# Performance work log

Hardware: AMD Instinct MI355X
Metric: run time of the kernel (lower is better)

## Reference

```python
import jax, jax.numpy as jnp
import numpy as np

B, NV, NC, D, E = 16, 8192, 4096, 128, 49152


def _gru_cell(x, h, w_ih, w_hh, b_ih, b_hh):
    """torch.nn.GRUCell math; gate order r, z, n; weights are (3D, D)."""
    gi = x @ w_ih.T + b_ih
    gh = h @ w_hh.T + b_hh
    ir, iz, inn = jnp.split(gi, 3, axis=-1)
    hr, hz, hn = jnp.split(gh, 3, axis=-1)
    r = jax.nn.sigmoid(ir + hr)
    z = jax.nn.sigmoid(iz + hz)
    n = jnp.tanh(inn + r * hn)
    return (1.0 - z) * n + z * h


def _msg_net(x, w1, b1, w2, b2):
    # Linear -> exact GELU -> Linear (torch nn.GELU default is erf-based)
    return jax.nn.gelu(x @ w1.T + b1, approximate=False) @ w2.T + b2


def _spmm(feats, src_idx, dst_idx, n_out):
    """Binary sparse-matrix @ dense: gather rows at src_idx, segment-sum to dst_idx.
    feats: (B, N_src, D) -> (B, n_out, D). Equivalent to torch.sparse.mm(H, feats[i])."""
    gathered = feats[:, src_idx, :]  # (B, E, D)
    return jax.vmap(lambda g: jax.ops.segment_sum(g, dst_idx, num_segments=n_out))(gathered)


def setup_inputs() -> dict:
    key = jax.random.key(0)
    ks = jax.random.split(key, 20)
    s = 0.05
    inp = {
        "v_feats": jax.random.normal(ks[0], (B, NV, D), jnp.float32),
        "c_feats": jax.random.normal(ks[1], (B, NC, D), jnp.float32),
        "edge_chk": jax.random.randint(ks[2], (E,), 0, NC, jnp.int32),
        "edge_var": jax.random.randint(ks[3], (E,), 0, NV, jnp.int32),
        # msg_net: Linear(D,D) -> GELU -> Linear(D,D)
        "msg_w1": jax.random.normal(ks[4], (D, D), jnp.float32) * s,
        "msg_b1": jnp.zeros((D,), jnp.float32),
        "msg_w2": jax.random.normal(ks[5], (D, D), jnp.float32) * s,
        "msg_b2": jnp.zeros((D,), jnp.float32),
        # var_update GRUCell(D, D)
        "var_w_ih": jax.random.normal(ks[6], (3 * D, D), jnp.float32) * s,
        "var_w_hh": jax.random.normal(ks[7], (3 * D, D), jnp.float32) * s,
        "var_b_ih": jnp.zeros((3 * D,), jnp.float32),
        "var_b_hh": jnp.zeros((3 * D,), jnp.float32),
        # chk_update GRUCell(D, D)
        "chk_w_ih": jax.random.normal(ks[8], (3 * D, D), jnp.float32) * s,
        "chk_w_hh": jax.random.normal(ks[9], (3 * D, D), jnp.float32) * s,
        "chk_b_ih": jnp.zeros((3 * D,), jnp.float32),
        "chk_b_hh": jnp.zeros((3 * D,), jnp.float32),
    }
    return inp


def reference(v_feats, c_feats, edge_chk, edge_var,
              msg_w1, msg_b1, msg_w2, msg_b2,
              var_w_ih, var_w_hh, var_b_ih, var_b_hh,
              chk_w_ih, chk_w_hh, chk_b_ih, chk_b_hh):
    b, nv, d = v_feats.shape
    nc = c_feats.shape[1]
    # variable -> check: H @ v_feats (H is binary, rows=checks, cols=vars)
    v_to_c = _spmm(v_feats, edge_var, edge_chk, nc)        # (B, NC, D)
    v_to_c = _msg_net(v_to_c, msg_w1, msg_b1, msg_w2, msg_b2)
    c_new = _gru_cell(v_to_c.reshape(-1, d), c_feats.reshape(-1, d),
                      chk_w_ih, chk_w_hh, chk_b_ih, chk_b_hh).reshape(b, nc, d)
    # check -> variable: H^T @ c_new
    c_to_v = _spmm(c_new, edge_chk, edge_var, nv)          # (B, NV, D)
    c_to_v = _msg_net(c_to_v, msg_w1, msg_b1, msg_w2, msg_b2)
    v_new = _gru_cell(c_to_v.reshape(-1, d), v_feats.reshape(-1, d),
                      var_w_ih, var_w_hh, var_b_ih, var_b_hh).reshape(b, nv, d)
    return (v_new, c_new)
```

## Files before the change

kernel.cpp:

```cpp
#include <hip/hip_runtime.h>

using u16 = unsigned short;
using u32 = unsigned int;
using u64 = unsigned long long;
typedef short short8 __attribute__((ext_vector_type(8)));
typedef unsigned short ushort8 __attribute__((ext_vector_type(8)));
typedef float f32x4 __attribute__((ext_vector_type(4)));

#define GB  16
#define GNV 8192
#define GNC 4096
#define GD  128
#define GE  49152

#define MFMA __builtin_amdgcn_mfma_f32_16x16x32_bf16


__device__ __forceinline__ u16 f2bf(float f){
    u32 u = __builtin_bit_cast(u32, f);
    u32 r = (u >> 16) & 1u;
    u += 0x7fffu + r;
    return (u16)(u >> 16);
}

__device__ __forceinline__ float bf2f(u16 x){
    return __builtin_bit_cast(float, (u32)x << 16);
}

__device__ __forceinline__ u64 pack4(float a, float b, float c, float d){
    return (u64)f2bf(a) | ((u64)f2bf(b) << 16) | ((u64)f2bf(c) << 32) | ((u64)f2bf(d) << 48);
}

__device__ __forceinline__ float sigmoidf_(float x){
    return __fdividef(1.f, 1.f + __expf(-x));
}

__device__ __forceinline__ float tanhf_fast(float x){
    float xc = fminf(15.f, fmaxf(-15.f, x));
    float t  = __expf(2.f * xc);
    return __fdividef(t - 1.f, t + 1.f);
}

__device__ __forceinline__ char* swzp(const void* base, int row, int bc){
    return (char*)base + row * 256 + (bc ^ ((row & 7) << 4));
}

__device__ __forceinline__ short8 ldfrag(const u16* tile, int row, int lane, int ks){
    int bc = ks * 64 + ((lane >> 4) << 4);
    return *(const short8*)swzp(tile, row, bc);
}


__global__ void k_hist(const int* __restrict__ ec, const int* __restrict__ ev,
                       int* cc, int* cv){
    int e = blockIdx.x * 256 + threadIdx.x;
    if (e < GE){ atomicAdd(&cc[ec[e]], 1); atomicAdd(&cv[ev[e]], 1); }
}

__global__ __launch_bounds__(1024) void k_scan(const int* __restrict__ cnt, int* off, int n){
    __shared__ int part[1024];
    int tid = threadIdx.x;
    int chunk = n >> 10;
    int base = tid * chunk;
    int s = 0;
    for (int i = 0; i < chunk; ++i) s += cnt[base + i];
    part[tid] = s;
    __syncthreads();
    #pragma unroll
    for (int ofs = 1; ofs < 1024; ofs <<= 1){
        int v = (tid >= ofs) ? part[tid - ofs] : 0;
        __syncthreads();
        part[tid] += v;
        __syncthreads();
    }
    if (tid == 1023) off[n] = part[1023];
    int run = part[tid] - s;
    for (int i = 0; i < chunk; ++i){ off[base + i] = run; run += cnt[base + i]; }
}

__global__ void k_fill(const int* __restrict__ ec, const int* __restrict__ ev,
                       int* cur_c, int* lst_c, int* cur_v, int* lst_v){
    int e = blockIdx.x * 256 + threadIdx.x;
    if (e < GE){
        int c = ec[e], v = ev[e];
        lst_c[atomicAdd(&cur_c[c], 1)] = v;
        lst_v[atomicAdd(&cur_v[v], 1)] = c;
    }
}

__global__ void k_sort(const int* __restrict__ off, int* lst, int n){
    int i = blockIdx.x * 256 + threadIdx.x;
    if (i >= n) return;
    int s = off[i], e = off[i + 1];
    for (int a = s + 1; a < e; ++a){
        int v = lst[a]; int b = a - 1;
        while (b >= s && lst[b] > v){ lst[b + 1] = lst[b]; --b; }
        lst[b + 1] = v;
    }
}

__global__ void k_cvt(const float* __restrict__ s, u16* d, int n){
    int i = blockIdx.x * 256 + threadIdx.x;
    if (i < n) d[i] = f2bf(s[i]);
}


__global__ __launch_bounds__(256) void k_tr(const float* __restrict__ src,
                                            u16* __restrict__ dstT, int n){
    const int node = blockIdx.x, t = threadIdx.x;
    const int b = t >> 4, d0 = (t & 15) * 8;
    const float4* s = (const float4*)(src + ((size_t)b * n + node) * GD + d0);
    float4 v0 = s[0], v1 = s[1];
    u64* p = (u64*)(dstT + (size_t)node * 2048 + t * 8);
    p[0] = pack4(v0.x, v0.y, v0.z, v0.w);
    p[1] = pack4(v1.x, v1.y, v1.z, v1.w);
}


__global__ __launch_bounds__(256) void k_spmm(const u16* __restrict__ srcT,
                                              const int* __restrict__ off,
                                              const int* __restrict__ lst,
                                              u16* __restrict__ dst, int ndst){
    const int node = blockIdx.x, t = threadIdx.x;
    const int b = t >> 4, d0 = (t & 15) * 8;
    float acc[8];
    #pragma unroll
    for (int i = 0; i < 8; ++i) acc[i] = 0.f;
    const int s = off[node], e = off[node + 1];
    const u16* base = srcT + t * 8;
    for (int a = s; a < e; ++a){
        ushort8 v = *(const ushort8*)(base + (size_t)lst[a] * 2048);
        #pragma unroll
        for (int i = 0; i < 8; ++i) acc[i] += bf2f(v[i]);
    }
    u64* p = (u64*)(dst + ((size_t)b * ndst + node) * GD + d0);
    p[0] = pack4(acc[0], acc[1], acc[2], acc[3]);
    p[1] = pack4(acc[4], acc[5], acc[6], acc[7]);
}


__global__ __launch_bounds__(512, 2) void k_msg(u16* __restrict__ X,
                                                const u16* __restrict__ W1, const float* __restrict__ b1,
                                                const u16* __restrict__ W2, const float* __restrict__ b2,
                                                int ntiles){
    __shared__ __align__(16) u16 Xs[2][64 * 128];
    __shared__ __align__(16) u16 Gs[64 * 128];
    const int tid = threadIdx.x, lane = tid & 63, w = tid >> 6;
    const int l15 = lane & 15, rg = lane >> 4;
    const int j = w * 16 + l15;

    short8 w1f[4], w2f[4];
    #pragma unroll
    for (int ks = 0; ks < 4; ++ks){
        w1f[ks] = *(const short8*)(W1 + (size_t)j * 128 + ks * 32 + rg * 8);
        w2f[ks] = *(const short8*)(W2 + (size_t)j * 128 + ks * 32 + rg * 8);
    }
    const float bb1 = b1[j], bb2 = b2[j];

    const int nk = ntiles / gridDim.x;
    u64 xr[4];
    auto issue = [&](int tt){
        const u64* xs = (const u64*)(X + (size_t)tt * 64 * 128);
        #pragma unroll
        for (int i = 0; i < 4; ++i) xr[i] = xs[tid + i * 512];
    };

    issue(blockIdx.x);
    for (int k = 0; k < nk; ++k){
        const int buf = k & 1;
        #pragma unroll
        for (int i = 0; i < 4; ++i){
            int idx = tid + i * 512;
            *(u64*)swzp(Xs[buf], idx >> 5, (idx & 31) << 3) = xr[i];
        }
        __syncthreads();
        if (k + 1 < nk) issue(blockIdx.x + (k + 1) * gridDim.x);

        #pragma unroll
        for (int sub = 0; sub < 4; ++sub){
            const u16* xt = Xs[buf] + sub * 16 * 128;
            f32x4 acc = {0, 0, 0, 0};
            #pragma unroll
            for (int ks = 0; ks < 4; ++ks)
                acc = MFMA(ldfrag(xt, l15, lane, ks), w1f[ks], acc, 0, 0, 0);
            #pragma unroll
            for (int i = 0; i < 4; ++i){
                float v = acc[i] + bb1;
                float g = 0.5f * v * (1.f + erff(v * 0.70710678f));
                *(u16*)swzp(Gs, sub * 16 + rg * 4 + i, j * 2) = f2bf(g);
            }
        }
        __syncthreads();

        const size_t row0 = (size_t)(blockIdx.x + (size_t)k * gridDim.x) * 64;
        #pragma unroll
        for (int sub = 0; sub < 4; ++sub){
            const u16* gt = Gs + sub * 16 * 128;
            f32x4 acc = {0, 0, 0, 0};
            #pragma unroll
            for (int ks = 0; ks < 4; ++ks)
                acc = MFMA(ldfrag(gt, l15, lane, ks), w2f[ks], acc, 0, 0, 0);
            #pragma unroll
            for (int i = 0; i < 4; ++i)
                X[(row0 + sub * 16 + rg * 4 + i) * GD + j] = f2bf(acc[i] + bb2);
        }
    }
}


__global__ __launch_bounds__(512, 2) void k_gru(const u16* __restrict__ Xb, const float* __restrict__ Hf,
                                                const u16* __restrict__ Wih, const float* __restrict__ bih,
                                                const u16* __restrict__ Whh, const float* __restrict__ bhh,
                                                float* __restrict__ Out, u16* __restrict__ OutT,
                                                int logN, int ntiles){
    __shared__ __align__(16) u16  Xs[2][64 * 128];
    __shared__ __align__(16) u16  Hs[2][64 * 128];
    __shared__ __align__(16) float Hraw[2][64 * 128];
    const int tid = threadIdx.x, lane = tid & 63, w = tid >> 6;
    const int l15 = lane & 15, rg = lane >> 4;
    const int j = w * 16 + l15;
    const int nmask = (1 << logN) - 1;

    short8 wf[6][4];
    #pragma unroll
    for (int g = 0; g < 3; ++g){
        #pragma unroll
        for (int ks = 0; ks < 4; ++ks){
            wf[g][ks]     = *(const short8*)(Wih + (size_t)(g * 128 + j) * 128 + ks * 32 + rg * 8);
            wf[g + 3][ks] = *(const short8*)(Whh + (size_t)(g * 128 + j) * 128 + ks * 32 + rg * 8);
        }
    }
    const float bir = bih[j]       + bhh[j];
    const float biz = bih[128 + j] + bhh[128 + j];
    const float bin = bih[256 + j];
    const float bhn = bhh[256 + j];

    const int nk = ntiles / gridDim.x;
    u64 xr[4]; float4 hr[4];

    auto issue = [&](int t){
        const u64*    xs = (const u64*)   (Xb + (size_t)t * 64 * 128);
        const float4* hs = (const float4*)(Hf + (size_t)t * 64 * 128);
        #pragma unroll
        for (int i = 0; i < 4; ++i){ xr[i] = xs[tid + i * 512]; hr[i] = hs[tid + i * 512]; }
    };

    issue(blockIdx.x);
    for (int k = 0; k < nk; ++k){
        const int buf = k & 1;
        #pragma unroll
        for (int i = 0; i < 4; ++i){
            int idx = tid + i * 512;
            int row = idx >> 5, c8 = idx & 31;
            *(u64*)swzp(Xs[buf], row, c8 << 3) = xr[i];
            float4 v = hr[i];
            *(float4*)&Hraw[buf][row * 128 + c8 * 4] = v;
            *(u64*)swzp(Hs[buf], row, c8 << 3) = pack4(v.x, v.y, v.z, v.w);
        }
        __syncthreads();
        if (k + 1 < nk) issue(blockIdx.x + (k + 1) * gridDim.x);

        const int row0 = (blockIdx.x + k * gridDim.x) * 64;
        #pragma unroll
        for (int sub = 0; sub < 4; ++sub){
            const u16* xt = Xs[buf] + sub * 16 * 128;
            const u16* ht = Hs[buf] + sub * 16 * 128;
            f32x4 ar = {0,0,0,0}, az = {0,0,0,0}, an = {0,0,0,0}, hn = {0,0,0,0};
            #pragma unroll
            for (int ks = 0; ks < 4; ++ks){
                short8 a = ldfrag(xt, l15, lane, ks);
                short8 h = ldfrag(ht, l15, lane, ks);
                ar = MFMA(a, wf[0][ks], ar, 0, 0, 0);
                az = MFMA(a, wf[1][ks], az, 0, 0, 0);
                an = MFMA(a, wf[2][ks], an, 0, 0, 0);
                ar = MFMA(h, wf[3][ks], ar, 0, 0, 0);
                az = MFMA(h, wf[4][ks], az, 0, 0, 0);
                hn = MFMA(h, wf[5][ks], hn, 0, 0, 0);
            }
            #pragma unroll
            for (int i = 0; i < 4; ++i){
                int r = sub * 16 + rg * 4 + i;
                float h0 = Hraw[buf][r * 128 + j];
                float rr = sigmoidf_(ar[i] + bir);
                float zz = sigmoidf_(az[i] + biz);
                float nn = tanhf_fast(an[i] + bin + rr * (hn[i] + bhn));
                float val = (1.f - zz) * nn + zz * h0;
                int rg_ = row0 + r;
                Out[(size_t)rg_ * GD + j] = val;
                if (OutT){
                    int bidx = rg_ >> logN, node = rg_ & nmask;
                    OutT[(((size_t)node << 4) + bidx) * GD + j] = f2bf(val);
                }
            }
        }
        __syncthreads();
    }
}


extern "C" void kernel_launch(void* const* d_in, const int* in_sizes, int n_in,
                              void* d_out, int out_size, void* d_ws, size_t ws_size,
                              hipStream_t stream){
    const float* v_feats  = (const float*)d_in[0];
    const float* c_feats  = (const float*)d_in[1];
    const int*   edge_chk = (const int*)d_in[2];
    const int*   edge_var = (const int*)d_in[3];
    const float* msg_w1   = (const float*)d_in[4];
    const float* msg_b1   = (const float*)d_in[5];
    const float* msg_w2   = (const float*)d_in[6];
    const float* msg_b2   = (const float*)d_in[7];
    const float* var_w_ih = (const float*)d_in[8];
    const float* var_w_hh = (const float*)d_in[9];
    const float* var_b_ih = (const float*)d_in[10];
    const float* var_b_hh = (const float*)d_in[11];
    const float* chk_w_ih = (const float*)d_in[12];
    const float* chk_w_hh = (const float*)d_in[13];
    const float* chk_b_ih = (const float*)d_in[14];
    const float* chk_b_hh = (const float*)d_in[15];

    float* out_v = (float*)d_out;
    float* out_c = out_v + (size_t)GB * GNV * GD;

    char* p = (char*)d_ws;
    auto take = [&](size_t bytes) -> void* {
        void* r = (void*)p; p += (bytes + 255) & ~(size_t)255; return r;
    };
    int* cnt_c = (int*)take(GNC * 4);
    int* cnt_v = (int*)take(GNV * 4);
    int* off_c = (int*)take((GNC + 1) * 4);
    int* off_v = (int*)take((GNV + 1) * 4);
    int* cur_c = (int*)take(GNC * 4);
    int* cur_v = (int*)take(GNV * 4);
    int* lst_c = (int*)take(GE * 4);
    int* lst_v = (int*)take(GE * 4);
    u16* w1b  = (u16*)take((size_t)GD * GD * 2);
    u16* w2b  = (u16*)take((size_t)GD * GD * 2);
    u16* cihb = (u16*)take((size_t)3 * GD * GD * 2);
    u16* chhb = (u16*)take((size_t)3 * GD * GD * 2);
    u16* vihb = (u16*)take((size_t)3 * GD * GD * 2);
    u16* vhhb = (u16*)take((size_t)3 * GD * GD * 2);
    u16* mc = (u16*)take((size_t)GB * GNC * GD * 2);
    u16* mv = (u16*)take((size_t)GB * GNV * GD * 2);
    u16* vT = (u16*)take((size_t)GNV * GB * GD * 2);
    u16* cT = (u16*)take((size_t)GNC * GB * GD * 2);

    hipMemsetAsync(cnt_c, 0, GNC * 4, stream);
    hipMemsetAsync(cnt_v, 0, GNV * 4, stream);
    k_hist<<<(GE + 255) / 256, 256, 0, stream>>>(edge_chk, edge_var, cnt_c, cnt_v);
    k_scan<<<1, 1024, 0, stream>>>(cnt_c, off_c, GNC);
    k_scan<<<1, 1024, 0, stream>>>(cnt_v, off_v, GNV);
    hipMemcpyAsync(cur_c, off_c, GNC * 4, hipMemcpyDeviceToDevice, stream);
    hipMemcpyAsync(cur_v, off_v, GNV * 4, hipMemcpyDeviceToDevice, stream);
    k_fill<<<(GE + 255) / 256, 256, 0, stream>>>(edge_chk, edge_var, cur_c, lst_c, cur_v, lst_v);
    k_sort<<<(GNC + 255) / 256, 256, 0, stream>>>(off_c, lst_c, GNC);
    k_sort<<<(GNV + 255) / 256, 256, 0, stream>>>(off_v, lst_v, GNV);

    k_cvt<<<(GD * GD + 255) / 256, 256, 0, stream>>>(msg_w1, w1b, GD * GD);
    k_cvt<<<(GD * GD + 255) / 256, 256, 0, stream>>>(msg_w2, w2b, GD * GD);
    k_cvt<<<(3 * GD * GD + 255) / 256, 256, 0, stream>>>(chk_w_ih, cihb, 3 * GD * GD);
    k_cvt<<<(3 * GD * GD + 255) / 256, 256, 0, stream>>>(chk_w_hh, chhb, 3 * GD * GD);
    k_cvt<<<(3 * GD * GD + 255) / 256, 256, 0, stream>>>(var_w_ih, vihb, 3 * GD * GD);
    k_cvt<<<(3 * GD * GD + 255) / 256, 256, 0, stream>>>(var_w_hh, vhhb, 3 * GD * GD);
    k_tr<<<GNV, 256, 0, stream>>>(v_feats, vT, GNV);

    k_spmm<<<GNC, 256, 0, stream>>>(vT, off_c, lst_c, mc, GNC);
    k_msg<<<256, 512, 0, stream>>>(mc, w1b, msg_b1, w2b, msg_b2, (GB * GNC) / 64);
    k_gru<<<256, 512, 0, stream>>>(mc, c_feats, cihb, chk_b_ih, chhb, chk_b_hh,
                                   out_c, cT, 12, (GB * GNC) / 64);
    k_spmm<<<GNV, 256, 0, stream>>>(cT, off_v, lst_v, mv, GNV);
    k_msg<<<256, 512, 0, stream>>>(mv, w1b, msg_b1, w2b, msg_b2, (GB * GNV) / 64);
    k_gru<<<256, 512, 0, stream>>>(mv, v_feats, vihb, var_b_ih, vhhb, var_b_hh,
                                   out_v, (u16*)nullptr, 13, (GB * GNV) / 64);
}
```

Baseline: 340.5 us.

## Deepen GRU kernel prefetch to two tiles, drop fp32 H staging in LDS

The GRU kernel now keeps two tiles of X/H loads in flight in registers, alternating buffers with one barrier per tile instead of two. It drops the fp32 Hraw LDS copy and re-reads h0 from global memory (likely cache-resident) in the epilogue. It also uses the hardware v_cvt_pk_bf16_f32 instruction for bf16 packing and issues wider 16-byte loads and stores. This cuts LDS footprint and conversion ALU work, at the cost of more registers and extra global reads. The loop assumes nk is even, and the second tile prefetch runs unconditionally even when nk is 1.

New measurement: 341.1 us. No clear change (+0.2%).

```diff
diff --git a/kernel.cpp b/kernel.cpp
--- a/kernel.cpp
+++ b/kernel.cpp
@@ -27,8 +27,14 @@
     return __builtin_bit_cast(float, (u32)x << 16);
 }
 
+__device__ __forceinline__ u32 cvtpk(float lo, float hi){
+    u32 r;
+    asm("v_cvt_pk_bf16_f32 %0, %1, %2" : "=v"(r) : "v"(lo), "v"(hi));
+    return r;
+}
+
 __device__ __forceinline__ u64 pack4(float a, float b, float c, float d){
-    return (u64)f2bf(a) | ((u64)f2bf(b) << 16) | ((u64)f2bf(c) << 32) | ((u64)f2bf(d) << 48);
+    return (u64)cvtpk(a, b) | ((u64)cvtpk(c, d) << 32);
 }
 
 __device__ __forceinline__ float sigmoidf_(float x){
@@ -213,9 +219,8 @@
                                                 const u16* __restrict__ Whh, const float* __restrict__ bhh,
                                                 float* __restrict__ Out, u16* __restrict__ OutT,
                                                 int logN, int ntiles){
-    __shared__ __align__(16) u16  Xs[2][64 * 128];
-    __shared__ __align__(16) u16  Hs[2][64 * 128];
-    __shared__ __align__(16) float Hraw[2][64 * 128];
+    __shared__ __align__(16) u16 Xs[2][64 * 128];
+    __shared__ __align__(16) u16 Hs[2][64 * 128];
     const int tid = threadIdx.x, lane = tid & 63, w = tid >> 6;
     const int l15 = lane & 15, rg = lane >> 4;
     const int j = w * 16 + l15;
@@ -236,35 +241,40 @@
     const float bhn = bhh[256 + j];
 
     const int nk = ntiles / gridDim.x;
-    u64 xr[4]; float4 hr[4];
-
-    auto issue = [&](int t){
-        const u64*    xs = (const u64*)   (Xb + (size_t)t * 64 * 128);
-        const float4* hs = (const float4*)(Hf + (size_t)t * 64 * 128);
-        #pragma unroll
-        for (int i = 0; i < 4; ++i){ xr[i] = xs[tid + i * 512]; hr[i] = hs[tid + i * 512]; }
-    };
-
-    issue(blockIdx.x);
-    for (int k = 0; k < nk; ++k){
-        const int buf = k & 1;
-        #pragma unroll
-        for (int i = 0; i < 4; ++i){
-            int idx = tid + i * 512;
-            int row = idx >> 5, c8 = idx & 31;
-            *(u64*)swzp(Xs[buf], row, c8 << 3) = xr[i];
-            float4 v = hr[i];
-            *(float4*)&Hraw[buf][row * 128 + c8 * 4] = v;
-            *(u64*)swzp(Hs[buf], row, c8 << 3) = pack4(v.x, v.y, v.z, v.w);
-        }
-        __syncthreads();
-        if (k + 1 < nk) issue(blockIdx.x + (k + 1) * gridDim.x);
-
-        const int row0 = (blockIdx.x + k * gridDim.x) * 64;
+    const int crow = (tid * 2) >> 4, cc = ((tid * 2) & 15) << 4;
+
+    ushort8 xrA[2], xrB[2]; float4 hrA[4], hrB[4];
+
+    auto issue = [&](ushort8* xr, float4* hr, int t){
+        const ushort8* xs = (const ushort8*)(Xb + (size_t)t * 8192) + tid * 2;
+        const float4*  hs = (const float4*) (Hf + (size_t)t * 8192) + tid * 4;
+        xr[0] = xs[0]; xr[1] = xs[1];
+        #pragma unroll
+        for (int i = 0; i < 4; ++i) hr[i] = hs[i];
+    };
+
+    auto commit = [&](const ushort8* xr, const float4* hr, int buf){
+        *(ushort8*)swzp(Xs[buf], crow, cc)      = xr[0];
+        *(ushort8*)swzp(Xs[buf], crow, cc + 16) = xr[1];
+        union { u32 u[4]; ushort8 v; } q0, q1;
+        q0.u[0] = cvtpk(hr[0].x, hr[0].y); q0.u[1] = cvtpk(hr[0].z, hr[0].w);
+        q0.u[2] = cvtpk(hr[1].x, hr[1].y); q0.u[3] = cvtpk(hr[1].z, hr[1].w);
+        q1.u[0] = cvtpk(hr[2].x, hr[2].y); q1.u[1] = cvtpk(hr[2].z, hr[2].w);
+        q1.u[2] = cvtpk(hr[3].x, hr[3].y); q1.u[3] = cvtpk(hr[3].z, hr[3].w);
+        *(ushort8*)swzp(Hs[buf], crow, cc)      = q0.v;
+        *(ushort8*)swzp(Hs[buf], crow, cc + 16) = q1.v;
+    };
+
+    auto compute = [&](int t, int buf){
+        const float* hg = Hf  + (size_t)t * 8192;
+        float*       og = Out + (size_t)t * 8192;
         #pragma unroll
         for (int sub = 0; sub < 4; ++sub){
-            const u16* xt = Xs[buf] + sub * 16 * 128;
-            const u16* ht = Hs[buf] + sub * 16 * 128;
+            const u16* xt = Xs[buf] + sub * 2048;
+            const u16* ht = Hs[buf] + sub * 2048;
+            float h0[4];
+            #pragma unroll
+            for (int i = 0; i < 4; ++i) h0[i] = hg[(sub * 16 + rg * 4 + i) * 128 + j];
             f32x4 ar = {0,0,0,0}, az = {0,0,0,0}, an = {0,0,0,0}, hn = {0,0,0,0};
             #pragma unroll
             for (int ks = 0; ks < 4; ++ks){
@@ -280,20 +290,34 @@
             #pragma unroll
             for (int i = 0; i < 4; ++i){
                 int r = sub * 16 + rg * 4 + i;
-                float h0 = Hraw[buf][r * 128 + j];
                 float rr = sigmoidf_(ar[i] + bir);
                 float zz = sigmoidf_(az[i] + biz);
                 float nn = tanhf_fast(an[i] + bin + rr * (hn[i] + bhn));
-                float val = (1.f - zz) * nn + zz * h0;
-                int rg_ = row0 + r;
-                Out[(size_t)rg_ * GD + j] = val;
+                float val = (1.f - zz) * nn + zz * h0[i];
+                og[r * 128 + j] = val;
                 if (OutT){
-                    int bidx = rg_ >> logN, node = rg_ & nmask;
+                    int grow = t * 64 + r;
+                    int bidx = grow >> logN, node = grow & nmask;
                     OutT[(((size_t)node << 4) + bidx) * GD + j] = f2bf(val);
                 }
             }
         }
-        __syncthreads();
+    };
+
+    issue(xrA, hrA, blockIdx.x);
+    issue(xrB, hrB, blockIdx.x + gridDim.x);
+    for (int k = 0; k < nk; k += 2){
+        const int t0 = blockIdx.x + k * gridDim.x;
+        commit(xrA, hrA, 0);
+        __syncthreads();
+        if (k + 2 < nk) issue(xrA, hrA, t0 + 2 * gridDim.x);
+        compute(t0, 0);
+
+        const int t1 = t0 + gridDim.x;
+        commit(xrB, hrB, 1);
+        __syncthreads();
+        if (k + 3 < nk) issue(xrB, hrB, t1 + 2 * gridDim.x);
+        compute(t1, 1);
     }
 }
 
```

## Store activations in MFMA fragment-native layout and drop LDS staging in GRU/msg

Applied to the files above, without the earlier changes.

Introduces a fragment-order layout (fidx) that spmm and transpose kernels write directly, so k_msg and k_gru can load MFMA A-operands straight from global memory without LDS staging and swizzled copies. The GRU hidden state is pre-converted to bf16 in that layout by an extra k_tr pass, and the old h0 comes from bf16 instead of fp32. GRU now software-pipelines two 16-row groups in registers, grids grow to 512 blocks, and packing uses v_cvt_pk_bf16_f32. The cost is an extra transpose pass over c_feats and lower precision for the h0 blend.

Result: slower. 432.6 us (+27.0%).

```diff
diff --git a/kernel.cpp b/kernel.cpp
--- a/kernel.cpp
+++ b/kernel.cpp
@@ -27,8 +27,14 @@
     return __builtin_bit_cast(float, (u32)x << 16);
 }
 
+__device__ __forceinline__ u32 cvtpk(float lo, float hi){
+    u32 r;
+    asm("v_cvt_pk_bf16_f32 %0, %1, %2" : "=v"(r) : "v"(lo), "v"(hi));
+    return r;
+}
+
 __device__ __forceinline__ u64 pack4(float a, float b, float c, float d){
-    return (u64)f2bf(a) | ((u64)f2bf(b) << 16) | ((u64)f2bf(c) << 32) | ((u64)f2bf(d) << 48);
+    return (u64)cvtpk(a, b) | ((u64)cvtpk(c, d) << 32);
 }
 
 __device__ __forceinline__ float sigmoidf_(float x){
@@ -39,6 +45,11 @@
     float xc = fminf(15.f, fmaxf(-15.f, x));
     float t  = __expf(2.f * xc);
     return __fdividef(t - 1.f, t + 1.f);
+}
+
+__device__ __forceinline__ size_t fidx(int r, int c){
+    return ((size_t)(r >> 4) << 11) + ((c >> 5) << 9)
+         + (((r & 15) + (((c & 31) >> 3) << 4)) << 3) + (c & 7);
 }
 
 __device__ __forceinline__ char* swzp(const void* base, int row, int bc){
@@ -106,21 +117,29 @@
 
 
 __global__ __launch_bounds__(256) void k_tr(const float* __restrict__ src,
-                                            u16* __restrict__ dstT, int n){
+                                            u16* __restrict__ dstT,
+                                            u16* __restrict__ dstF, int n){
     const int node = blockIdx.x, t = threadIdx.x;
     const int b = t >> 4, d0 = (t & 15) * 8;
     const float4* s = (const float4*)(src + ((size_t)b * n + node) * GD + d0);
     float4 v0 = s[0], v1 = s[1];
-    u64* p = (u64*)(dstT + (size_t)node * 2048 + t * 8);
-    p[0] = pack4(v0.x, v0.y, v0.z, v0.w);
-    p[1] = pack4(v1.x, v1.y, v1.z, v1.w);
+    u64 lo = pack4(v0.x, v0.y, v0.z, v0.w);
+    u64 hi = pack4(v1.x, v1.y, v1.z, v1.w);
+    if (dstT){
+        u64* p = (u64*)(dstT + (size_t)node * 2048 + t * 8);
+        p[0] = lo; p[1] = hi;
+    }
+    if (dstF){
+        u64* q = (u64*)(dstF + fidx(b * n + node, d0));
+        q[0] = lo; q[1] = hi;
+    }
 }
 
 
 __global__ __launch_bounds__(256) void k_spmm(const u16* __restrict__ srcT,
                                               const int* __restrict__ off,
                                               const int* __restrict__ lst,
-                                              u16* __restrict__ dst, int ndst){
+                                              u16* __restrict__ dstF, int ndst){
     const int node = blockIdx.x, t = threadIdx.x;
     const int b = t >> 4, d0 = (t & 15) * 8;
     float acc[8];
@@ -133,17 +152,16 @@
         #pragma unroll
         for (int i = 0; i < 8; ++i) acc[i] += bf2f(v[i]);
     }
-    u64* p = (u64*)(dst + ((size_t)b * ndst + node) * GD + d0);
+    u64* p = (u64*)(dstF + fidx(b * ndst + node, d0));
     p[0] = pack4(acc[0], acc[1], acc[2], acc[3]);
     p[1] = pack4(acc[4], acc[5], acc[6], acc[7]);
 }
 
 
-__global__ __launch_bounds__(512, 2) void k_msg(u16* __restrict__ X,
-                                                const u16* __restrict__ W1, const float* __restrict__ b1,
-                                                const u16* __restrict__ W2, const float* __restrict__ b2,
-                                                int ntiles){
-    __shared__ __align__(16) u16 Xs[2][64 * 128];
+__global__ __launch_bounds__(512) void k_msg(u16* __restrict__ X,
+                                             const u16* __restrict__ W1, const float* __restrict__ b1,
+                                             const u16* __restrict__ W2, const float* __restrict__ b2,
+                                             int ntiles){
     __shared__ __align__(16) u16 Gs[64 * 128];
     const int tid = threadIdx.x, lane = tid & 63, w = tid >> 6;
     const int l15 = lane & 15, rg = lane >> 4;
@@ -158,31 +176,17 @@
     const float bb1 = b1[j], bb2 = b2[j];
 
     const int nk = ntiles / gridDim.x;
-    u64 xr[4];
-    auto issue = [&](int tt){
-        const u64* xs = (const u64*)(X + (size_t)tt * 64 * 128);
-        #pragma unroll
-        for (int i = 0; i < 4; ++i) xr[i] = xs[tid + i * 512];
-    };
-
-    issue(blockIdx.x);
     for (int k = 0; k < nk; ++k){
-        const int buf = k & 1;
-        #pragma unroll
-        for (int i = 0; i < 4; ++i){
-            int idx = tid + i * 512;
-            *(u64*)swzp(Xs[buf], idx >> 5, (idx & 31) << 3) = xr[i];
-        }
-        __syncthreads();
-        if (k + 1 < nk) issue(blockIdx.x + (k + 1) * gridDim.x);
+        const int t = blockIdx.x + k * gridDim.x;
+        const u16* xb = X + ((size_t)t << 13);
 
         #pragma unroll
         for (int sub = 0; sub < 4; ++sub){
-            const u16* xt = Xs[buf] + sub * 16 * 128;
+            const u16* gb = xb + (sub << 11);
             f32x4 acc = {0, 0, 0, 0};
             #pragma unroll
             for (int ks = 0; ks < 4; ++ks)
-                acc = MFMA(ldfrag(xt, l15, lane, ks), w1f[ks], acc, 0, 0, 0);
+                acc = MFMA(*(const short8*)(gb + ks * 512 + lane * 8), w1f[ks], acc, 0, 0, 0);
             #pragma unroll
             for (int i = 0; i < 4; ++i){
                 float v = acc[i] + bb1;
@@ -192,30 +196,27 @@
         }
         __syncthreads();
 
-        const size_t row0 = (size_t)(blockIdx.x + (size_t)k * gridDim.x) * 64;
         #pragma unroll
         for (int sub = 0; sub < 4; ++sub){
-            const u16* gt = Gs + sub * 16 * 128;
+            const u16* gt = Gs + sub * 2048;
             f32x4 acc = {0, 0, 0, 0};
             #pragma unroll
             for (int ks = 0; ks < 4; ++ks)
                 acc = MFMA(ldfrag(gt, l15, lane, ks), w2f[ks], acc, 0, 0, 0);
             #pragma unroll
             for (int i = 0; i < 4; ++i)
-                X[(row0 + sub * 16 + rg * 4 + i) * GD + j] = f2bf(acc[i] + bb2);
-        }
-    }
-}
-
-
-__global__ __launch_bounds__(512, 2) void k_gru(const u16* __restrict__ Xb, const float* __restrict__ Hf,
-                                                const u16* __restrict__ Wih, const float* __restrict__ bih,
-                                                const u16* __restrict__ Whh, const float* __restrict__ bhh,
-                                                float* __restrict__ Out, u16* __restrict__ OutT,
-                                                int logN, int ntiles){
-    __shared__ __align__(16) u16  Xs[2][64 * 128];
-    __shared__ __align__(16) u16  Hs[2][64 * 128];
-    __shared__ __align__(16) float Hraw[2][64 * 128];
+                X[fidx(t * 64 + sub * 16 + rg * 4 + i, j)] = f2bf(acc[i] + bb2);
+        }
+        __syncthreads();
+    }
+}
+
+
+__global__ __launch_bounds__(512) void k_gru(const u16* __restrict__ XF, const u16* __restrict__ HF,
+                                             const u16* __restrict__ Wih, const float* __restrict__ bih,
+                                             const u16* __restrict__ Whh, const float* __restrict__ bhh,
+                                             float* __restrict__ Out, u16* __restrict__ OutT,
+                                             int logN, int ngroups){
     const int tid = threadIdx.x, lane = tid & 63, w = tid >> 6;
     const int l15 = lane & 15, rg = lane >> 4;
     const int j = w * 16 + l15;
@@ -235,65 +236,60 @@
     const float bin = bih[256 + j];
     const float bhn = bhh[256 + j];
 
-    const int nk = ntiles / gridDim.x;
-    u64 xr[4]; float4 hr[4];
-
-    auto issue = [&](int t){
-        const u64*    xs = (const u64*)   (Xb + (size_t)t * 64 * 128);
-        const float4* hs = (const float4*)(Hf + (size_t)t * 64 * 128);
-        #pragma unroll
-        for (int i = 0; i < 4; ++i){ xr[i] = xs[tid + i * 512]; hr[i] = hs[tid + i * 512]; }
+    const int h0off = ((j >> 5) << 9) + (((j & 31) >> 3) << 7) + ((rg * 4) << 3) + (j & 7);
+
+    const int stride = gridDim.x;
+    const int ng = ngroups / stride;
+
+    short8 xfA[4], hfA[4], xfB[4], hfB[4];
+    float h0A[4], h0B[4];
+
+    auto load = [&](short8* xf, short8* hf, float* h0, int g){
+        const u16* xb = XF + ((size_t)g << 11);
+        const u16* hb = HF + ((size_t)g << 11);
+        #pragma unroll
+        for (int ks = 0; ks < 4; ++ks){
+            xf[ks] = *(const short8*)(xb + ks * 512 + lane * 8);
+            hf[ks] = *(const short8*)(hb + ks * 512 + lane * 8);
+        }
+        #pragma unroll
+        for (int i = 0; i < 4; ++i) h0[i] = bf2f(hb[h0off + i * 8]);
     };
 
-    issue(blockIdx.x);
-    for (int k = 0; k < nk; ++k){
-        const int buf = k & 1;
+    auto comp = [&](const short8* xf, const short8* hf, const float* h0, int g){
+        f32x4 ar = {0,0,0,0}, az = {0,0,0,0}, an = {0,0,0,0}, hn = {0,0,0,0};
+        #pragma unroll
+        for (int ks = 0; ks < 4; ++ks){
+            ar = MFMA(xf[ks], wf[0][ks], ar, 0, 0, 0);
+            az = MFMA(xf[ks], wf[1][ks], az, 0, 0, 0);
+            an = MFMA(xf[ks], wf[2][ks], an, 0, 0, 0);
+            ar = MFMA(hf[ks], wf[3][ks], ar, 0, 0, 0);
+            az = MFMA(hf[ks], wf[4][ks], az, 0, 0, 0);
+            hn = MFMA(hf[ks], wf[5][ks], hn, 0, 0, 0);
+        }
         #pragma unroll
         for (int i = 0; i < 4; ++i){
-            int idx = tid + i * 512;
-            int row = idx >> 5, c8 = idx & 31;
-            *(u64*)swzp(Xs[buf], row, c8 << 3) = xr[i];
-            float4 v = hr[i];
-            *(float4*)&Hraw[buf][row * 128 + c8 * 4] = v;
-            *(u64*)swzp(Hs[buf], row, c8 << 3) = pack4(v.x, v.y, v.z, v.w);
-        }
-        __syncthreads();
-        if (k + 1 < nk) issue(blockIdx.x + (k + 1) * gridDim.x);
-
-        const int row0 = (blockIdx.x + k * gridDim.x) * 64;
-        #pragma unroll
-        for (int sub = 0; sub < 4; ++sub){
-            const u16* xt = Xs[buf] + sub * 16 * 128;
-            const u16* ht = Hs[buf] + sub * 16 * 128;
-            f32x4 ar = {0,0,0,0}, az = {0,0,0,0}, an = {0,0,0,0}, hn = {0,0,0,0};
-            #pragma unroll
-            for (int ks = 0; ks < 4; ++ks){
-                short8 a = ldfrag(xt, l15, lane, ks);
-                short8 h = ldfrag(ht, l15, lane, ks);
-                ar = MFMA(a, wf[0][ks], ar, 0, 0, 0);
-                az = MFMA(a, wf[1][ks], az, 0, 0, 0);
-                an = MFMA(a, wf[2][ks], an, 0, 0, 0);
-                ar = MFMA(h, wf[3][ks], ar, 0, 0, 0);
-                az = MFMA(h, wf[4][ks], az, 0, 0, 0);
-                hn = MFMA(h, wf[5][ks], hn, 0, 0, 0);
+            int r = g * 16 + rg * 4 + i;
+            float rr = sigmoidf_(ar[i] + bir);
+            float zz = sigmoidf_(az[i] + biz);
+            float nn = tanhf_fast(an[i] + bin + rr * (hn[i] + bhn));
+            float val = (1.f - zz) * nn + zz * h0[i];
+            Out[(size_t)r * GD + j] = val;
+            if (OutT){
+                int bidx = r >> logN, node = r & nmask;
+                OutT[(((size_t)node << 4) + bidx) * GD + j] = f2bf(val);
             }
-            #pragma unroll
-            for (int i = 0; i < 4; ++i){
-                int r = sub * 16 + rg * 4 + i;
-                float h0 = Hraw[buf][r * 128 + j];
-                float rr = sigmoidf_(ar[i] + bir);
-                float zz = sigmoidf_(az[i] + biz);
-                float nn = tanhf_fast(an[i] + bin + rr * (hn[i] + bhn));
-                float val = (1.f - zz) * nn + zz * h0;
-                int rg_ = row0 + r;
-                Out[(size_t)rg_ * GD + j] = val;
-                if (OutT){
-                    int bidx = rg_ >> logN, node = rg_ & nmask;
-                    OutT[(((size_t)node << 4) + bidx) * GD + j] = f2bf(val);
-                }
-            }
-        }
-        __syncthreads();
+        }
+    };
+
+    int g = blockIdx.x;
+    load(xfA, hfA, h0A, g);
+    for (int k = 0; k < ng; k += 2){
+        load(xfB, hfB, h0B, g + stride);
+        comp(xfA, hfA, h0A, g);
+        if (k + 2 < ng) load(xfA, hfA, h0A, g + 2 * stride);
+        comp(xfB, hfB, h0B, g + stride);
+        g += 2 * stride;
     }
 }
 
@@ -343,6 +339,8 @@
     u16* mv = (u16*)take((size_t)GB * GNV * GD * 2);
     u16* vT = (u16*)take((size_t)GNV * GB * GD * 2);
     u16* cT = (u16*)take((size_t)GNC * GB * GD * 2);
+    u16* vF = (u16*)take((size_t)GB * GNV * GD * 2);
+    u16* cF = (u16*)take((size_t)GB * GNC * GD * 2);
 
     hipMemsetAsync(cnt_c, 0, GNC * 4, stream);
     hipMemsetAsync(cnt_v, 0, GNV * 4, stream);
@@ -361,14 +359,15 @@
     k_cvt<<<(3 * GD * GD + 255) / 256, 256, 0, stream>>>(chk_w_hh, chhb, 3 * GD * GD);
     k_cvt<<<(3 * GD * GD + 255) / 256, 256, 0, stream>>>(var_w_ih, vihb, 3 * GD * GD);
     k_cvt<<<(3 * GD * GD + 255) / 256, 256, 0, stream>>>(var_w_hh, vhhb, 3 * GD * GD);
-    k_tr<<<GNV, 256, 0, stream>>>(v_feats, vT, GNV);
+    k_tr<<<GNV, 256, 0, stream>>>(v_feats, vT, vF, GNV);
+    k_tr<<<GNC, 256, 0, stream>>>(c_feats, (u16*)nullptr, cF, GNC);
 
     k_spmm<<<GNC, 256, 0, stream>>>(vT, off_c, lst_c, mc, GNC);
-    k_msg<<<256, 512, 0, stream>>>(mc, w1b, msg_b1, w2b, msg_b2, (GB * GNC) / 64);
-    k_gru<<<256, 512, 0, stream>>>(mc, c_feats, cihb, chk_b_ih, chhb, chk_b_hh,
-                                   out_c, cT, 12, (GB * GNC) / 64);
+    k_msg<<<512, 512, 0, stream>>>(mc, w1b, msg_b1, w2b, msg_b2, (GB * GNC) / 64);
+    k_gru<<<512, 512, 0, stream>>>(mc, cF, cihb, chk_b_ih, chhb, chk_b_hh,
+                                   out_c, cT, 12, (GB * GNC) / 16);
     k_spmm<<<GNV, 256, 0, stream>>>(cT, off_v, lst_v, mv, GNV);
-    k_msg<<<256, 512, 0, stream>>>(mv, w1b, msg_b1, w2b, msg_b2, (GB * GNV) / 64);
-    k_gru<<<256, 512, 0, stream>>>(mv, v_feats, vihb, var_b_ih, vhhb, var_b_hh,
-                                   out_v, (u16*)nullptr, 13, (GB * GNV) / 64);
-}
+    k_msg<<<512, 512, 0, stream>>>(mv, w1b, msg_b1, w2b, msg_b2, (GB * GNV) / 64);
+    k_gru<<<512, 512, 0, stream>>>(mv, vF, vihb, var_b_ih, vhhb, var_b_hh,
+                                   out_v, (u16*)nullptr, 13, (GB * GNV) / 16);
+}
```
